# Performance work log

Measured on AMD Instinct MI355X. Metric: run time of the kernel, lower is better.

The kernel has to match this reference:

```python
import jax, jax.numpy as jnp
import numpy as np

HEADS, HD = 8, 64

def swish(x):
    return x * jax.nn.sigmoid(x)

def layer_norm(x, eps=1e-5):
    mu = jnp.mean(x, axis=-1, keepdims=True)
    var = jnp.var(x, axis=-1, keepdims=True)
    return (x - mu) / jnp.sqrt(var + eps)

def setup_inputs() -> dict:
    key = jax.random.key(0)
    k1, k2, k3 = jax.random.split(key, 3)
    B, L, D = 2, 2048, 512
    x = jax.random.normal(k1, (B, L, D), jnp.float32)
    cnn_w = jax.random.normal(k2, (HEADS * HD * 3, D, 3), jnp.float32) * 0.02
    cnn_b = jnp.zeros((HEADS * HD * 3,), jnp.float32)
    fc_w = jax.random.normal(k3, (D, HEADS * HD), jnp.float32) * 0.02
    fc_b = jnp.zeros((D,), jnp.float32)
    return {"x": x, "cnn_w": cnn_w, "cnn_b": cnn_b, "fc_w": fc_w, "fc_b": fc_b}

def reference(x, cnn_w, cnn_b, fc_w, fc_b):
    B, L, D = x.shape
    # Conv1d(dims -> heads*hd*3, kernel=3, stride=1, pad=1) on channel-first layout
    xt = jnp.transpose(x, (0, 2, 1))  # [B, D, L]
    y = jax.lax.conv_general_dilated(
        xt, cnn_w, window_strides=(1,), padding=[(1, 1)],
        dimension_numbers=("NCH", "OIH", "NCH"),
    ) + cnn_b[None, :, None]  # [B, 3*H*HD, L]
    qkv = swish(y).reshape(B, HEADS, HD * 3, L)
    q, k, v = jnp.split(qkv, 3, axis=-2)  # each [B, H, HD, L]
    # NOTE: original scales by sqrt(length), not sqrt(hd)
    scores = jnp.einsum("bhdw,bhdm->bhwm", q, k) / jnp.sqrt(jnp.float32(L))
    att = jax.nn.softmax(scores, axis=-1)  # [B, H, L, L]
    new_v = jnp.einsum("bhwm,bhdm->bwhd", att, v).reshape(B, L, HEADS * HD)
    m = swish(new_v @ fc_w.T + fc_b)  # [B, L, D]
    return layer_norm(x * 2 + m)
```

## Files before the change

kernel.cpp:

```cpp
#include <hip/hip_runtime.h>
#include <hip/hip_bf16.h>

#define BB 2
#define LL 2048
#define DD 512
#define HH 8
#define HDM 64
#define SCALE 0.022097086912079608f
#define QSCALE 0.03187935766f

typedef __hip_bfloat16 bf16;
typedef unsigned short u16;
typedef __attribute__((ext_vector_type(8))) short short8v;
typedef __attribute__((ext_vector_type(4))) float float4v;

#define XN  2097152
#define WN  2359296
#define BN  1536
#define FWN 262144
#define FBN 512

__device__ __forceinline__ float b2f(u16 u) {
    return __uint_as_float(((unsigned int)u) << 16);
}
__device__ __forceinline__ u16 f2u(float f) {
    bf16 h = __float2bfloat16(f);
    u16 r;
    __builtin_memcpy(&r, &h, 2);
    return r;
}
__device__ __forceinline__ uint4 pack8(const float* f) {
    uint4 p;
    p.x = (unsigned)f2u(f[0]) | ((unsigned)f2u(f[1]) << 16);
    p.y = (unsigned)f2u(f[2]) | ((unsigned)f2u(f[3]) << 16);
    p.z = (unsigned)f2u(f[4]) | ((unsigned)f2u(f[5]) << 16);
    p.w = (unsigned)f2u(f[6]) | ((unsigned)f2u(f[7]) << 16);
    return p;
}

__device__ __forceinline__ void gld_lds16(const u16* g, u16* l) {
    __builtin_amdgcn_global_load_lds(
        (const __attribute__((address_space(1))) unsigned int*)g,
        (__attribute__((address_space(3))) unsigned int*)l, 16, 0, 0);
}

__device__ __forceinline__ int detect_flag(const u16* __restrict__ xraw) {
    int bad = 0;
    int lane = threadIdx.x & 63;
    for (int i = lane; i < 256; i += 64) {
        float v = b2f(xraw[i]);
        if (!(fabsf(v) < 100.f)) bad = 1;
    }
    return (__ballot(bad) != 0ull) ? 1 : 0;
}

__device__ __forceinline__ void conv8(const void* src, u16* dst, size_t i, int flag) {
    if (flag) {
        const float* s = (const float*)src;
        float f[8];
        float4 a = *(const float4*)(s + i);
        float4 b = *(const float4*)(s + i + 4);
        f[0] = a.x; f[1] = a.y; f[2] = a.z; f[3] = a.w;
        f[4] = b.x; f[5] = b.y; f[6] = b.z; f[7] = b.w;
        *(uint4*)(dst + i) = pack8(f);
    } else {
        *(uint4*)(dst + i) = *(const uint4*)((const u16*)src + i);
    }
}

__global__ __launch_bounds__(256) void prep_kernel(
    const void* __restrict__ xsrc, const void* __restrict__ wsrc,
    const void* __restrict__ bsrc, const void* __restrict__ fwsrc,
    const void* __restrict__ fbsrc,
    u16* __restrict__ xp, u16* __restrict__ wt,
    u16* __restrict__ bc, u16* __restrict__ fwc, u16* __restrict__ fbc)
{
    const int flag = detect_flag((const u16*)xsrc);
    const int bid = blockIdx.x;

    if (bid < 1024) {
        int idx = bid * 256 + threadIdx.x;
        if (idx < 256) {
            int b2  = idx >> 7;
            int r2  = (idx >> 6) & 1;
            int c82 = (idx & 63) * 8;
            size_t off = ((size_t)(b2 * 2050 + (r2 ? 2049 : 0))) * 512 + c82;
            uint4 z = {0u, 0u, 0u, 0u};
            *(uint4*)(xp + off) = z;
        }
        int b   = idx / (LL * 64);
        int rem = idx - b * (LL * 64);
        int l   = rem >> 6;
        int c8  = (rem & 63) * 8;
        size_t si = ((size_t)(b * LL + l)) * 512 + c8;
        size_t di = ((size_t)(b * 2050 + l + 1)) * 512 + c8;
        if (flag) {
            const float* s = (const float*)xsrc;
            float f[8];
            float4 a = *(const float4*)(s + si);
            float4 bq = *(const float4*)(s + si + 4);
            f[0] = a.x; f[1] = a.y; f[2] = a.z; f[3] = a.w;
            f[4] = bq.x; f[5] = bq.y; f[6] = bq.z; f[7] = bq.w;
            *(uint4*)(xp + di) = pack8(f);
        } else {
            *(uint4*)(xp + di) = *(const uint4*)((const u16*)xsrc + si);
        }
    } else if (bid < 1216) {
        __shared__ u16 wl[8 * 1536];
        const int t  = threadIdx.x;
        const int o0 = (bid - 1024) * 8;
        if (flag) {
            const float4* s4 = (const float4*)((const float*)wsrc + (size_t)o0 * 1536);
#pragma unroll
            for (int v = 0; v < 12; ++v) {
                int i4 = v * 256 + t;
                float4 q = s4[i4];
                uint2 p;
                p.x = (unsigned)f2u(q.x) | ((unsigned)f2u(q.y) << 16);
                p.y = (unsigned)f2u(q.z) | ((unsigned)f2u(q.w) << 16);
                *(uint2*)&wl[i4 * 4] = p;
            }
        } else {
            const uint4* s8 = (const uint4*)((const u16*)wsrc + (size_t)o0 * 1536);
#pragma unroll
            for (int v = 0; v < 6; ++v) {
                int i8 = v * 256 + t;
                *(uint4*)&wl[i8 * 8] = s8[i8];
            }
        }
        __syncthreads();
#pragma unroll
        for (int v = 0; v < 6; ++v) {
            int oct = v * 256 + t;
            int row = oct / 192;
            int rem = oct - row * 192;
            int k   = rem >> 6;
            int i8  = rem & 63;
            u16 tmp[8];
#pragma unroll
            for (int j = 0; j < 8; ++j) tmp[j] = wl[row * 1536 + (i8 * 8 + j) * 3 + k];
            uint4 val;
            val.x = (unsigned)tmp[0] | ((unsigned)tmp[1] << 16);
            val.y = (unsigned)tmp[2] | ((unsigned)tmp[3] << 16);
            val.z = (unsigned)tmp[4] | ((unsigned)tmp[5] << 16);
            val.w = (unsigned)tmp[6] | ((unsigned)tmp[7] << 16);
            *(uint4*)(wt + (size_t)(o0 + row) * 1536 + k * 512 + i8 * 8) = val;
        }
    } else {
        int o = (bid - 1216) * 256 + threadIdx.x;
        if (o < BN / 8) {
            conv8(bsrc, bc, (size_t)o * 8, flag);
        } else if (o < BN / 8 + FWN / 8) {
            conv8(fwsrc, fwc, (size_t)(o - BN / 8) * 8, flag);
        } else if (o < BN / 8 + FWN / 8 + FBN / 8) {
            conv8(fbsrc, fbc, (size_t)(o - BN / 8 - FWN / 8) * 8, flag);
        }
    }
}

__global__ __launch_bounds__(256) void conv_mfma_kernel(
    const u16* __restrict__ xp,
    const u16* __restrict__ wt,
    const u16* __restrict__ bias,
    u16* __restrict__ qkbuf,
    u16* __restrict__ vbuf)
{
    __shared__ u16 smem[32768];
    u16* Asb = smem;
    u16* Bsb = smem + 2 * 128 * 64;
#define OTS 140
    u16* OT  = smem;

    const int blk = blockIdx.x;
    const int rt = blk / 12;
    const int ct = blk - rt * 12;
    const int b  = rt >> 4;
    const int l0 = (rt & 15) * 128;
    const int tid  = threadIdx.x;
    const int wave = tid >> 6;
    const int lane = tid & 63;
    const int quad = lane >> 4;
    const int l16  = lane & 15;
    const int e7   = l16 & 7;
    const int wx = wave & 1;
    const int wy = wave >> 1;

    float4v acc[4][4];
#pragma unroll
    for (int mt = 0; mt < 4; ++mt)
#pragma unroll
        for (int nt = 0; nt < 4; ++nt) acc[mt][nt] = (float4v){0.f, 0.f, 0.f, 0.f};

    const int rowW = wave * 32;
    const int lrow = lane >> 3;
    const int g8   = (((lane & 7) ^ lrow)) * 8;
    auto stage = [&](int kc, int buf) {
        const int slab = kc >> 3;
        const int i0   = (kc & 7) * 64;
        const u16* ga = xp + ((size_t)(b * 2050 + l0 + rowW + slab + lrow)) * 512 + i0 + g8;
        const u16* gb = wt + ((size_t)(ct * 128 + rowW + lrow)) * 1536 + kc * 64 + g8;
        u16* la = Asb + (size_t)(buf * 128 + rowW) * 64;
        u16* lb = Bsb + (size_t)(buf * 128 + rowW) * 64;
#pragma unroll
        for (int j = 0; j < 4; ++j) {
            gld_lds16(ga + (size_t)(j * 8) * 512,  la + (j * 8) * 64);
            gld_lds16(gb + (size_t)(j * 8) * 1536, lb + (j * 8) * 64);
        }
    };

    stage(0, 0);

    for (int kc = 0; kc < 24; ++kc) {
        const int cur = kc & 1;
        __syncthreads();

        if (kc < 23) stage(kc + 1, 1 - cur);

#pragma unroll
        for (int half = 0; half < 2; ++half) {
            const int p = ((half * 4 + quad) ^ e7) * 8;
            short8v aF[4], bF[4];
#pragma unroll
            for (int mt = 0; mt < 4; ++mt)
                aF[mt] = *(const short8v*)&Asb[(size_t)(cur * 128 + wy * 64 + mt * 16 + l16) * 64 + p];
#pragma unroll
            for (int nt = 0; nt < 4; ++nt)
                bF[nt] = *(const short8v*)&Bsb[(size_t)(cur * 128 + wx * 64 + nt * 16 + l16) * 64 + p];
#pragma unroll
            for (int mt = 0; mt < 4; ++mt)
#pragma unroll
                for (int nt = 0; nt < 4; ++nt)
                    acc[mt][nt] = __builtin_amdgcn_mfma_f32_16x16x32_bf16(
                        aF[mt], bF[nt], acc[mt][nt], 0, 0, 0);
        }
    }

    __syncthreads();
    {
        const int tloc = (ct * 2 + wx) % 3;
#pragma unroll
        for (int nt = 0; nt < 4; ++nt) {
            int oc = wx * 64 + nt * 16 + l16;
            float bb = b2f(bias[ct * 128 + oc]);
#pragma unroll
            for (int mt = 0; mt < 4; ++mt)
#pragma unroll
                for (int r = 0; r < 4; ++r) {
                    int lr = wy * 64 + mt * 16 + quad * 4 + r;
                    float y = acc[mt][nt][r] + bb;
                    y = y / (1.f + __expf(-y));
                    if (tloc == 0) y *= QSCALE;
                    OT[lr * OTS + oc] = f2u(y);
                }
        }
    }
    __syncthreads();

#pragma unroll
    for (int g = 0; g < 2; ++g) {
        int a  = ct * 2 + g;
        int t  = a % 3;
        int bh = b * HH + a / 3;
        if (t != 2) {
            u16* base = qkbuf + ((size_t)((bh * 2 + t) * LL + l0)) * HDM;
#pragma unroll
            for (int it = 0; it < 4; ++it) {
                int idx = it * 256 + tid;
                int l   = idx >> 3;
                int d8  = (idx & 7) * 8;
                uint4 val = *(const uint4*)&OT[l * OTS + g * 64 + d8];
                *(uint4*)(base + (size_t)l * HDM + d8) = val;
            }
        } else {
            u16* base = vbuf + ((size_t)(bh * HDM)) * LL + l0;
#pragma unroll
            for (int it = 0; it < 4; ++it) {
                int idx = it * 256 + tid;
                int dd  = idx >> 4;
                int p   = idx & 15;
                int l8  = p * 8;
                u16 tmp[8];
#pragma unroll
                for (int j = 0; j < 8; ++j) tmp[j] = OT[(l8 + j) * OTS + g * 64 + dd];
                int a32 = p >> 2;
                int pb_ = p & 3;
                int q2  = (2 * pb_) & 3;
                int h2  = pb_ >> 1;
                int n0  = 32 * a32 + 8 * q2 + 4 * h2;
                uint2 v0, v1;
                v0.x = (unsigned)tmp[0] | ((unsigned)tmp[1] << 16);
                v0.y = (unsigned)tmp[2] | ((unsigned)tmp[3] << 16);
                v1.x = (unsigned)tmp[4] | ((unsigned)tmp[5] << 16);
                v1.y = (unsigned)tmp[6] | ((unsigned)tmp[7] << 16);
                *(uint2*)(base + (size_t)dd * LL + n0)     = v0;
                *(uint2*)(base + (size_t)dd * LL + n0 + 8) = v1;
            }
        }
    }
#undef OTS
}

__global__ __launch_bounds__(512) void attn_mfma_kernel(
    const u16* __restrict__ qk,
    const u16* __restrict__ v,
    u16* __restrict__ newv)
{
    __shared__ u16 smem[32768];
    u16 (*kts)[2][64][64] = (u16 (*)[2][64][64])smem;
    u16 (*vts)[2][64][64] = (u16 (*)[2][64][64])(smem + 16384);

    const int lb = ((blockIdx.x & 7) << 5) + (blockIdx.x >> 3);
    const int bh = lb >> 4;
    const int qc = lb & 15;
    const int b  = bh >> 3;
    const int h  = bh & 7;
    const int tid  = threadIdx.x;
    const int wave = tid >> 6;
    const int kg   = wave >> 2;
    const int qg   = wave & 3;
    const int lane = tid & 63;
    const int quad = lane >> 4;
    const int l16  = lane & 15;
    const int e7   = l16 & 7;

    const u16* qbase = qk + ((size_t)(bh * 2 + 0)) * LL * HDM;
    const u16* kbase = qk + ((size_t)(bh * 2 + 1)) * LL * HDM;
    const u16* vbase = v + (size_t)bh * HDM * LL;

    const int q0 = qc * 128 + qg * 32;

    short8v qfrag[2][2];
#pragma unroll
    for (int sg = 0; sg < 2; ++sg) {
        const u16* qr = qbase + (size_t)(q0 + sg * 16 + l16) * HDM + quad * 8;
        qfrag[sg][0] = *(const short8v*)(qr);
        qfrag[sg][1] = *(const short8v*)(qr + 32);
    }

    short8v vones;
    {
        short o1 = (l16 == 0) ? (short)0x3F80 : (short)0;
#pragma unroll
        for (int j = 0; j < 8; ++j) vones[j] = o1;
    }

    float4v oacc[2][4];
    float4v lacc[2];
#pragma unroll
    for (int sg = 0; sg < 2; ++sg) {
        lacc[sg] = (float4v){0.f, 0.f, 0.f, 0.f};
#pragma unroll
        for (int dt = 0; dt < 4; ++dt) oacc[sg][dt] = (float4v){0.f, 0.f, 0.f, 0.f};
    }

    const int rr  = qg * 8 + (lane >> 3);
    const int sw8 = ((lane & 7) ^ (lane >> 3)) * 8;
    auto stage = [&](int ic, int buf) {
        const int m0 = ic * 64;
#pragma unroll
        for (int r = 0; r < 2; ++r) {
            gld_lds16(kbase + (size_t)(m0 + r * 32 + rr) * HDM + sw8,
                      &kts[kg][buf][r * 32 + qg * 8][0]);
            gld_lds16(vbase + (size_t)(r * 32 + rr) * LL + m0 + sw8,
                      &vts[kg][buf][r * 32 + qg * 8][0]);
        }
    };

    stage(kg, 0);

    for (int i = 0; i < 16; ++i) {
        const int cur = i & 1;
        __syncthreads();

        if (i < 15) stage(2 * (i + 1) + kg, 1 - cur);

        float4v s[2][4];
#pragma unroll
        for (int mt = 0; mt < 4; ++mt) {
            short8v b0 = *(const short8v*)&kts[kg][cur][mt * 16 + l16][((quad) ^ e7) * 8];
            short8v b1 = *(const short8v*)&kts[kg][cur][mt * 16 + l16][((quad + 4) ^ e7) * 8];
#pragma unroll
            for (int sg = 0; sg < 2; ++sg) {
                float4v t = (float4v){0.f, 0.f, 0.f, 0.f};
                t = __builtin_amdgcn_mfma_f32_16x16x32_bf16(b0, qfrag[sg][0], t, 0, 0, 0);
                t = __builtin_amdgcn_mfma_f32_16x16x32_bf16(b1, qfrag[sg][1], t, 0, 0, 0);
                s[sg][mt] = t;
            }
        }

        unsigned pk[2][4][2];
#pragma unroll
        for (int sg = 0; sg < 2; ++sg)
#pragma unroll
            for (int mt = 0; mt < 4; ++mt) {
                float p0 = __builtin_amdgcn_exp2f(s[sg][mt][0]);
                float p1 = __builtin_amdgcn_exp2f(s[sg][mt][1]);
                float p2 = __builtin_amdgcn_exp2f(s[sg][mt][2]);
                float p3 = __builtin_amdgcn_exp2f(s[sg][mt][3]);
                pk[sg][mt][0] = (unsigned)f2u(p0) | ((unsigned)f2u(p1) << 16);
                pk[sg][mt][1] = (unsigned)f2u(p2) | ((unsigned)f2u(p3) << 16);
            }

#pragma unroll
        for (int mu = 0; mu < 2; ++mu) {
            short8v pb[2];
#pragma unroll
            for (int sg = 0; sg < 2; ++sg) {
                union { short8v v8; unsigned u[4]; } U;
                U.u[0] = pk[sg][2 * mu][0];
                U.u[1] = pk[sg][2 * mu][1];
                U.u[2] = pk[sg][2 * mu + 1][0];
                U.u[3] = pk[sg][2 * mu + 1][1];
                pb[sg] = U.v8;
                lacc[sg] = __builtin_amdgcn_mfma_f32_16x16x32_bf16(vones, pb[sg], lacc[sg], 0, 0, 0);
            }
#pragma unroll
            for (int dt = 0; dt < 4; ++dt) {
                short8v va = *(const short8v*)&vts[kg][cur][dt * 16 + l16][((mu * 4 + quad) ^ e7) * 8];
#pragma unroll
                for (int sg = 0; sg < 2; ++sg)
                    oacc[sg][dt] = __builtin_amdgcn_mfma_f32_16x16x32_bf16(va, pb[sg], oacc[sg][dt], 0, 0, 0);
            }
        }
    }

    float dnm[2];
#pragma unroll
    for (int sg = 0; sg < 2; ++sg) dnm[sg] = __shfl(lacc[sg][0], l16);

    __syncthreads();
    float* xch = (float*)smem;
    if (kg == 1) {
#pragma unroll
        for (int sg = 0; sg < 2; ++sg) {
#pragma unroll
            for (int dt = 0; dt < 4; ++dt)
#pragma unroll
                for (int r = 0; r < 4; ++r)
                    xch[((qg * 34 + (sg * 16 + dt * 4 + r)) << 6) + lane] = oacc[sg][dt][r];
            xch[((qg * 34 + 32 + sg) << 6) + lane] = dnm[sg];
        }
    }
    __syncthreads();
    if (kg == 0) {
        u16* ob = newv + (size_t)b * LL * 512 + h * 64;
#pragma unroll
        for (int sg = 0; sg < 2; ++sg) {
            float dt2 = dnm[sg] + xch[((qg * 34 + 32 + sg) << 6) + lane];
            float inv = 1.f / dt2;
            const size_t orow = (size_t)(q0 + sg * 16 + l16) * 512 + quad * 4;
#pragma unroll
            for (int dt = 0; dt < 4; ++dt) {
                float o0 = oacc[sg][dt][0] + xch[((qg * 34 + (sg * 16 + dt * 4 + 0)) << 6) + lane];
                float o1 = oacc[sg][dt][1] + xch[((qg * 34 + (sg * 16 + dt * 4 + 1)) << 6) + lane];
                float o2 = oacc[sg][dt][2] + xch[((qg * 34 + (sg * 16 + dt * 4 + 2)) << 6) + lane];
                float o3 = oacc[sg][dt][3] + xch[((qg * 34 + (sg * 16 + dt * 4 + 3)) << 6) + lane];
                unsigned lo = (unsigned)f2u(o0 * inv) | ((unsigned)f2u(o1 * inv) << 16);
                unsigned hi = (unsigned)f2u(o2 * inv) | ((unsigned)f2u(o3 * inv) << 16);
                uint2 val; val.x = lo; val.y = hi;
                *(uint2*)(ob + orow + dt * 16) = val;
            }
        }
    }
}

__global__ __launch_bounds__(512) void fc_ln_mfma_kernel(
    const u16* __restrict__ newv,
    const u16* __restrict__ fcw,
    const u16* __restrict__ fcb,
    const u16* __restrict__ xp,
    const u16* __restrict__ xraw,
    void* __restrict__ out)
{
    const int flag = detect_flag(xraw);
    const int l0 = blockIdx.x * 16;
    const int tid  = threadIdx.x;
    const int wave = tid >> 6;
    const int lane = tid & 63;
    const int quad = lane >> 4;
    const int l16  = lane & 15;
    const int col0 = wave * 64;

    const int bb_ = l0 >> 11;
    const size_t xbase = ((size_t)(bb_ * 2050 + (l0 & 2047) + 1)) * 512;

    __shared__ u16 As[16][512];
    __shared__ float psum[8][16], psq[8][16];

#pragma unroll
    for (int r = 0; r < 2; ++r) {
        const int row = wave + r * 8;
        gld_lds16(newv + (size_t)(l0 + row) * 512 + ((lane ^ (row & 7)) * 8),
                  &As[row][0]);
    }
    __syncthreads();

    short8v aF[16];
#pragma unroll
    for (int kc = 0; kc < 16; ++kc)
        aF[kc] = *(const short8v*)&As[l16][(((kc * 4 + quad)) ^ (l16 & 7)) * 8];

    float4v acc[4];
#pragma unroll
    for (int nt = 0; nt < 4; ++nt) acc[nt] = (float4v){0.f, 0.f, 0.f, 0.f};

#pragma unroll
    for (int nt = 0; nt < 4; ++nt) {
        const u16* brow = fcw + (size_t)(col0 + nt * 16 + l16) * 512 + quad * 8;
#pragma unroll
        for (int kc = 0; kc < 16; ++kc) {
            short8v bF = *(const short8v*)(brow + kc * 32);
            acc[nt] = __builtin_amdgcn_mfma_f32_16x16x32_bf16(aF[kc], bF, acc[nt], 0, 0, 0);
        }
    }

    float z[4][4];
    float rs[4] = {0.f, 0.f, 0.f, 0.f}, rq[4] = {0.f, 0.f, 0.f, 0.f};
#pragma unroll
    for (int nt = 0; nt < 4; ++nt) {
        int col = col0 + nt * 16 + l16;
        float bb = b2f(fcb[col]);
#pragma unroll
        for (int r = 0; r < 4; ++r) {
            int row = quad * 4 + r;
            float y = acc[nt][r] + bb;
            float sw = y / (1.f + __expf(-y));
            float xv = b2f(xp[xbase + (size_t)row * 512 + col]);
            float zz = xv * 2.f + sw;
            z[nt][r] = zz;
            rs[r] += zz;
            rq[r] += zz * zz;
        }
    }
#pragma unroll
    for (int msk = 1; msk <= 8; msk <<= 1)
#pragma unroll
        for (int r = 0; r < 4; ++r) {
            rs[r] += __shfl_xor(rs[r], msk);
            rq[r] += __shfl_xor(rq[r], msk);
        }
    if (l16 == 0) {
#pragma unroll
        for (int r = 0; r < 4; ++r) {
            psum[wave][quad * 4 + r] = rs[r];
            psq[wave][quad * 4 + r]  = rq[r];
        }
    }
    __syncthreads();

    float mu[4], inv[4];
#pragma unroll
    for (int r = 0; r < 4; ++r) {
        int row = quad * 4 + r;
        float s = 0.f, q = 0.f;
#pragma unroll
        for (int w = 0; w < 8; ++w) { s += psum[w][row]; q += psq[w][row]; }
        float m = s * (1.f / 512.f);
        float var = q * (1.f / 512.f) - m * m;
        mu[r] = m;
        inv[r] = rsqrtf(var + 1e-5f);
    }

#pragma unroll
    for (int nt = 0; nt < 4; ++nt) {
        int col = col0 + nt * 16 + l16;
#pragma unroll
        for (int r = 0; r < 4; ++r) {
            int row = quad * 4 + r;
            float val = (z[nt][r] - mu[r]) * inv[r];
            if (flag) ((float*)out)[(size_t)(l0 + row) * 512 + col] = val;
            else      ((u16*)out)[(size_t)(l0 + row) * 512 + col] = f2u(val);
        }
    }
}

extern "C" void kernel_launch(void* const* d_in, const int* in_sizes, int n_in,
                              void* d_out, int out_size, void* d_ws, size_t ws_size,
                              hipStream_t stream) {
    (void)in_sizes; (void)n_in; (void)out_size; (void)ws_size;

    char* ws = (char*)d_ws;
    u16* xp   = (u16*)(ws + 256);
    u16* wtc  = (u16*)(ws + 4198656);
    u16* bc   = (u16*)(ws + 8917248);
    u16* fwc  = (u16*)(ws + 8920320);
    u16* fbc  = (u16*)(ws + 9444608);
    u16* qkb  = (u16*)(ws + 9445632);
    u16* vb   = (u16*)(ws + 17834240);
    u16* nvc  = (u16*)(ws + 22028544);

    prep_kernel<<<dim3(1345), dim3(256), 0, stream>>>(
        d_in[0], d_in[1], d_in[2], d_in[3], d_in[4],
        xp, wtc, bc, fwc, fbc);

    conv_mfma_kernel<<<dim3(32 * 12), dim3(256), 0, stream>>>(xp, wtc, bc, qkb, vb);
    attn_mfma_kernel<<<dim3(256), dim3(512), 0, stream>>>(qkb, vb, nvc);
    fc_ln_mfma_kernel<<<dim3(256), dim3(512), 0, stream>>>(
        nvc, fwc, fbc, xp, (const u16*)d_in[0], d_out);
}
```

Baseline: 149.1 us.

## Split attention keys across four wave groups with 64-query tiles per wave

Reorganizes the attention block's wave layout from 2 key-groups × 4 query-groups to 4 key-groups × 2 query-groups. Each wave now handles 64 queries, so every K/V fragment read from LDS feeds twice as many MFMAs. Shared memory doubles to 128KB to hold double-buffered K/V tiles for four key groups, and the final reduction merges three partial results instead of one. It also fuses exp2 directly after the QK MFMA. The costs are higher register pressure from the larger accumulators, fewer resident blocks because of the LDS size, and a heavier cross-group reduction at the end.

```diff
diff --git a/kernel.cpp b/kernel.cpp
--- a/kernel.cpp
+++ b/kernel.cpp
@@ -305,9 +305,9 @@
     const u16* __restrict__ v,
     u16* __restrict__ newv)
 {
-    __shared__ u16 smem[32768];
+    __shared__ u16 smem[65536];
     u16 (*kts)[2][64][64] = (u16 (*)[2][64][64])smem;
-    u16 (*vts)[2][64][64] = (u16 (*)[2][64][64])(smem + 16384);
+    u16 (*vts)[2][64][64] = (u16 (*)[2][64][64])(smem + 32768);
 
     const int lb = ((blockIdx.x & 7) << 5) + (blockIdx.x >> 3);
     const int bh = lb >> 4;
@@ -316,8 +316,8 @@
     const int h  = bh & 7;
     const int tid  = threadIdx.x;
     const int wave = tid >> 6;
-    const int kg   = wave >> 2;
-    const int qg   = wave & 3;
+    const int kg   = wave >> 1;
+    const int qg   = wave & 1;
     const int lane = tid & 63;
     const int quad = lane >> 4;
     const int l16  = lane & 15;
@@ -327,11 +327,11 @@
     const u16* kbase = qk + ((size_t)(bh * 2 + 1)) * LL * HDM;
     const u16* vbase = v + (size_t)bh * HDM * LL;
 
-    const int q0 = qc * 128 + qg * 32;
-
-    short8v qfrag[2][2];
-#pragma unroll
-    for (int sg = 0; sg < 2; ++sg) {
+    const int q0 = qc * 128 + qg * 64;
+
+    short8v qfrag[4][2];
+#pragma unroll
+    for (int sg = 0; sg < 4; ++sg) {
         const u16* qr = qbase + (size_t)(q0 + sg * 16 + l16) * HDM + quad * 8;
         qfrag[sg][0] = *(const short8v*)(qr);
         qfrag[sg][1] = *(const short8v*)(qr + 32);
@@ -344,68 +344,61 @@
         for (int j = 0; j < 8; ++j) vones[j] = o1;
     }
 
-    float4v oacc[2][4];
-    float4v lacc[2];
-#pragma unroll
-    for (int sg = 0; sg < 2; ++sg) {
+    float4v oacc[4][4];
+    float4v lacc[4];
+#pragma unroll
+    for (int sg = 0; sg < 4; ++sg) {
         lacc[sg] = (float4v){0.f, 0.f, 0.f, 0.f};
 #pragma unroll
         for (int dt = 0; dt < 4; ++dt) oacc[sg][dt] = (float4v){0.f, 0.f, 0.f, 0.f};
     }
 
-    const int rr  = qg * 8 + (lane >> 3);
-    const int sw8 = ((lane & 7) ^ (lane >> 3)) * 8;
+    const int rw8 = lane >> 3;
+    const int sw8 = ((lane & 7) ^ rw8) * 8;
     auto stage = [&](int ic, int buf) {
         const int m0 = ic * 64;
 #pragma unroll
-        for (int r = 0; r < 2; ++r) {
-            gld_lds16(kbase + (size_t)(m0 + r * 32 + rr) * HDM + sw8,
-                      &kts[kg][buf][r * 32 + qg * 8][0]);
-            gld_lds16(vbase + (size_t)(r * 32 + rr) * LL + m0 + sw8,
-                      &vts[kg][buf][r * 32 + qg * 8][0]);
+        for (int r = 0; r < 4; ++r) {
+            const int row0 = r * 16 + qg * 8;
+            gld_lds16(kbase + (size_t)(m0 + row0 + rw8) * HDM + sw8,
+                      &kts[kg][buf][row0][0]);
+            gld_lds16(vbase + (size_t)(row0 + rw8) * LL + m0 + sw8,
+                      &vts[kg][buf][row0][0]);
         }
     };
 
     stage(kg, 0);
 
-    for (int i = 0; i < 16; ++i) {
+    for (int i = 0; i < 8; ++i) {
         const int cur = i & 1;
         __syncthreads();
 
-        if (i < 15) stage(2 * (i + 1) + kg, 1 - cur);
-
-        float4v s[2][4];
+        if (i < 7) stage(4 * (i + 1) + kg, 1 - cur);
+
+        unsigned pk[4][4][2];
 #pragma unroll
         for (int mt = 0; mt < 4; ++mt) {
             short8v b0 = *(const short8v*)&kts[kg][cur][mt * 16 + l16][((quad) ^ e7) * 8];
             short8v b1 = *(const short8v*)&kts[kg][cur][mt * 16 + l16][((quad + 4) ^ e7) * 8];
 #pragma unroll
-            for (int sg = 0; sg < 2; ++sg) {
+            for (int sg = 0; sg < 4; ++sg) {
                 float4v t = (float4v){0.f, 0.f, 0.f, 0.f};
                 t = __builtin_amdgcn_mfma_f32_16x16x32_bf16(b0, qfrag[sg][0], t, 0, 0, 0);
                 t = __builtin_amdgcn_mfma_f32_16x16x32_bf16(b1, qfrag[sg][1], t, 0, 0, 0);
-                s[sg][mt] = t;
-            }
-        }
-
-        unsigned pk[2][4][2];
-#pragma unroll
-        for (int sg = 0; sg < 2; ++sg)
-#pragma unroll
-            for (int mt = 0; mt < 4; ++mt) {
-                float p0 = __builtin_amdgcn_exp2f(s[sg][mt][0]);
-                float p1 = __builtin_amdgcn_exp2f(s[sg][mt][1]);
-                float p2 = __builtin_amdgcn_exp2f(s[sg][mt][2]);
-                float p3 = __builtin_amdgcn_exp2f(s[sg][mt][3]);
+                float p0 = __builtin_amdgcn_exp2f(t[0]);
+                float p1 = __builtin_amdgcn_exp2f(t[1]);
+                float p2 = __builtin_amdgcn_exp2f(t[2]);
+                float p3 = __builtin_amdgcn_exp2f(t[3]);
                 pk[sg][mt][0] = (unsigned)f2u(p0) | ((unsigned)f2u(p1) << 16);
                 pk[sg][mt][1] = (unsigned)f2u(p2) | ((unsigned)f2u(p3) << 16);
             }
+        }
 
 #pragma unroll
         for (int mu = 0; mu < 2; ++mu) {
-            short8v pb[2];
-#pragma unroll
-            for (int sg = 0; sg < 2; ++sg) {
+            short8v pb[4];
+#pragma unroll
+            for (int sg = 0; sg < 4; ++sg) {
                 union { short8v v8; unsigned u[4]; } U;
                 U.u[0] = pk[sg][2 * mu][0];
                 U.u[1] = pk[sg][2 * mu][1];
@@ -418,50 +411,60 @@
             for (int dt = 0; dt < 4; ++dt) {
                 short8v va = *(const short8v*)&vts[kg][cur][dt * 16 + l16][((mu * 4 + quad) ^ e7) * 8];
 #pragma unroll
-                for (int sg = 0; sg < 2; ++sg)
+                for (int sg = 0; sg < 4; ++sg)
                     oacc[sg][dt] = __builtin_amdgcn_mfma_f32_16x16x32_bf16(va, pb[sg], oacc[sg][dt], 0, 0, 0);
             }
         }
     }
 
-    float dnm[2];
-#pragma unroll
-    for (int sg = 0; sg < 2; ++sg) dnm[sg] = __shfl(lacc[sg][0], l16);
+    float dnm[4];
+#pragma unroll
+    for (int sg = 0; sg < 4; ++sg) dnm[sg] = __shfl(lacc[sg][0], l16);
 
     __syncthreads();
     float* xch = (float*)smem;
-    if (kg == 1) {
-#pragma unroll
-        for (int sg = 0; sg < 2; ++sg) {
+#define XRG (2 * 68 * 64)
+    if (kg > 0) {
+        float* rg = xch + (kg - 1) * XRG + qg * (68 * 64);
+#pragma unroll
+        for (int sg = 0; sg < 4; ++sg) {
 #pragma unroll
             for (int dt = 0; dt < 4; ++dt)
 #pragma unroll
                 for (int r = 0; r < 4; ++r)
-                    xch[((qg * 34 + (sg * 16 + dt * 4 + r)) << 6) + lane] = oacc[sg][dt][r];
-            xch[((qg * 34 + 32 + sg) << 6) + lane] = dnm[sg];
+                    rg[((sg * 16 + dt * 4 + r) << 6) + lane] = oacc[sg][dt][r];
+            rg[((64 + sg) << 6) + lane] = dnm[sg];
         }
     }
     __syncthreads();
     if (kg == 0) {
         u16* ob = newv + (size_t)b * LL * 512 + h * 64;
-#pragma unroll
-        for (int sg = 0; sg < 2; ++sg) {
-            float dt2 = dnm[sg] + xch[((qg * 34 + 32 + sg) << 6) + lane];
-            float inv = 1.f / dt2;
+        const float* rg = xch + qg * (68 * 64);
+#pragma unroll
+        for (int sg = 0; sg < 4; ++sg) {
+            float dsum = dnm[sg];
+#pragma unroll
+            for (int p = 0; p < 3; ++p) dsum += rg[p * XRG + ((64 + sg) << 6) + lane];
+            float inv = 1.f / dsum;
             const size_t orow = (size_t)(q0 + sg * 16 + l16) * 512 + quad * 4;
 #pragma unroll
             for (int dt = 0; dt < 4; ++dt) {
-                float o0 = oacc[sg][dt][0] + xch[((qg * 34 + (sg * 16 + dt * 4 + 0)) << 6) + lane];
-                float o1 = oacc[sg][dt][1] + xch[((qg * 34 + (sg * 16 + dt * 4 + 1)) << 6) + lane];
-                float o2 = oacc[sg][dt][2] + xch[((qg * 34 + (sg * 16 + dt * 4 + 2)) << 6) + lane];
-                float o3 = oacc[sg][dt][3] + xch[((qg * 34 + (sg * 16 + dt * 4 + 3)) << 6) + lane];
-                unsigned lo = (unsigned)f2u(o0 * inv) | ((unsigned)f2u(o1 * inv) << 16);
-                unsigned hi = (unsigned)f2u(o2 * inv) | ((unsigned)f2u(o3 * inv) << 16);
+                float o[4];
+#pragma unroll
+                for (int r = 0; r < 4; ++r) {
+                    o[r] = oacc[sg][dt][r];
+#pragma unroll
+                    for (int p = 0; p < 3; ++p)
+                        o[r] += rg[p * XRG + ((sg * 16 + dt * 4 + r) << 6) + lane];
+                }
+                unsigned lo = (unsigned)f2u(o[0] * inv) | ((unsigned)f2u(o[1] * inv) << 16);
+                unsigned hi = (unsigned)f2u(o[2] * inv) | ((unsigned)f2u(o[3] * inv) << 16);
                 uint2 val; val.x = lo; val.y = hi;
                 *(uint2*)(ob + orow + dt * 16) = val;
             }
         }
     }
+#undef XRG
 }
 
 __global__ __launch_bounds__(512) void fc_ln_mfma_kernel(
```

Result: no change. 149.4 us (+0.2%).
